# Kernel tuning notes

Hardware: AMD Instinct MI355X
Metric: run time of the kernel (lower is better)

Reference implementation:

```python
import jax, jax.numpy as jnp
import numpy as np

B, T, V = 4, 4096, 1024
NB = 64          # n_basis -> basis dim = 2*NB
C = 256          # n_channels


def setup_inputs() -> dict:
    key = jax.random.key(0)
    ks = jax.random.split(key, 8)
    return {
        "x": jax.random.normal(ks[0], (B, T, V), dtype=jnp.float32),
        "basis": jax.random.normal(ks[1], (V, 2 * NB), dtype=jnp.float32),
        "q_coeffs": jax.random.normal(ks[2], (C, 2 * NB), dtype=jnp.float32) * 0.02,
        "k_coeffs": jax.random.normal(ks[3], (C, 2 * NB), dtype=jnp.float32) * 0.02,
        "v_coeffs": jax.random.normal(ks[4], (C, 2 * NB), dtype=jnp.float32) * 0.02,
        "o_coeffs": jax.random.normal(ks[5], (C, 2 * NB), dtype=jnp.float32) * 0.02,
        "decay_logit": jnp.float32(3.0),
        "out_scale": jnp.float32(0.1),
    }


def reference(x, basis, q_coeffs, k_coeffs, v_coeffs, o_coeffs, decay_logit, out_scale):
    # Fourier projections: [V, 2NB] @ [2NB, C] -> [V, C]
    q_w = basis @ q_coeffs.T
    k_w = basis @ k_coeffs.T
    v_w = basis @ v_coeffs.T
    o_w = basis @ o_coeffs.T

    queries = x @ q_w   # [B,T,C]
    keys = x @ k_w      # [B,T,C]
    values = x @ v_w    # [B,T,C]

    scores = jnp.einsum("btc,bsc->bts", queries, keys)  # [B,T,T]

    decay = jax.nn.sigmoid(decay_logit)
    t = x.shape[1]
    pos = jnp.arange(t)
    diff = pos[None, :] - pos[:, None]          # diff[s,t] = t - s (matches torch)
    causal = (diff > 0).astype(x.dtype)
    decay_weights = (decay ** jnp.maximum(diff - 1, 0).astype(x.dtype)) * causal

    scores = scores * decay_weights[None]       # [B,T,T]
    retrieved = jnp.einsum("bts,bsc->btc", scores, values)  # [B,T,C]
    return (retrieved @ o_w.T) * out_scale      # [B,T,V]
```

## Files before the change

### kernel.cpp

```cpp
#include <hip/hip_runtime.h>


#define Bb 4
#define Tt 4096
#define Vv 1024
#define Ff 128
#define Cc 256
#define TC 64
#define Gg (Tt / TC)
#define QLD 768

typedef __attribute__((ext_vector_type(8))) short short8;
typedef __attribute__((ext_vector_type(4))) float f32x4;

__device__ __forceinline__ float dsigmoid(const float* p) {
    return 1.0f / (1.0f + expf(-p[0]));
}
__device__ __forceinline__ ushort f2bf(float f) {
    unsigned u = __float_as_uint(f);
    u = (u + 0x7FFFu + ((u >> 16) & 1u)) >> 16;
    return (ushort)u;
}
__device__ __forceinline__ float bf2f(ushort u) {
    return __uint_as_float(((unsigned)u) << 16);
}

__global__ __launch_bounds__(256) void prep_weights(
    const float* __restrict__ basis, const float* __restrict__ qc,
    const float* __restrict__ kc, const float* __restrict__ vc,
    const float* __restrict__ oc,
    ushort* __restrict__ basisTb,
    ushort* __restrict__ qkvc,
    ushort* __restrict__ ocb)
{
    int i = blockIdx.x * 256 + threadIdx.x;
    if (i < Ff * Vv) {
        int f = i >> 10, v = i & 1023;
        basisTb[i] = f2bf(basis[v * Ff + f]);
    }
    if (i < 768 * Ff) {
        int ch = i >> 7, f = i & 127;
        const float* src = ch < 256 ? qc : (ch < 512 ? kc : vc);
        qkvc[i] = f2bf(src[(ch & 255) * Ff + f]);
    }
    if (i < Cc * Ff) ocb[i] = f2bf(oc[i]);
}

template<int AMODE, int OMODE>
__global__ __launch_bounds__(256) void mgemm(
    const void* __restrict__ Ap, const ushort* __restrict__ Bt,
    void* __restrict__ Cp, int N_total, int K_total, int ldA, int Ksplit,
    const float* __restrict__ alpha_ptr)
{
    __shared__ ushort Asm[128][40];
    __shared__ ushort Bsm[128][40];
    const int tid = threadIdx.x;
    const int row0 = blockIdx.x * 128;
    const int col0 = blockIdx.y * 128;
    const int kb = blockIdx.z * Ksplit;

    const int trow = tid >> 1;
    const int thalf = (tid & 1) * 16;

    const int l = tid & 63, w = tid >> 6;
    const int wr = (w >> 1) * 64, wc = (w & 1) * 64;
    const int lrow = l & 15, lk = l >> 4;

    f32x4 acc[4][4];
#pragma unroll
    for (int mi = 0; mi < 4; ++mi)
#pragma unroll
        for (int ni = 0; ni < 4; ++ni) {
            f32x4 z = {0.f, 0.f, 0.f, 0.f};
            acc[mi][ni] = z;
        }

    for (int k0 = kb; k0 < kb + Ksplit; k0 += 32) {
        if (AMODE == 1) {
            const float* ap = (const float*)Ap + (size_t)(row0 + trow) * ldA + k0 + thalf;
            float4 f0 = ((const float4*)ap)[0];
            float4 f1 = ((const float4*)ap)[1];
            float4 f2 = ((const float4*)ap)[2];
            float4 f3 = ((const float4*)ap)[3];
            union { ushort us[16]; int4 i4[2]; } t;
            t.us[0] = f2bf(f0.x); t.us[1] = f2bf(f0.y); t.us[2] = f2bf(f0.z); t.us[3] = f2bf(f0.w);
            t.us[4] = f2bf(f1.x); t.us[5] = f2bf(f1.y); t.us[6] = f2bf(f1.z); t.us[7] = f2bf(f1.w);
            t.us[8] = f2bf(f2.x); t.us[9] = f2bf(f2.y); t.us[10] = f2bf(f2.z); t.us[11] = f2bf(f2.w);
            t.us[12] = f2bf(f3.x); t.us[13] = f2bf(f3.y); t.us[14] = f2bf(f3.z); t.us[15] = f2bf(f3.w);
            *(int4*)&Asm[trow][thalf] = t.i4[0];
            *(int4*)&Asm[trow][thalf + 8] = t.i4[1];
        } else {
            const ushort* ap = (const ushort*)Ap + (size_t)(row0 + trow) * ldA + k0 + thalf;
            *(int4*)&Asm[trow][thalf] = ((const int4*)ap)[0];
            *(int4*)&Asm[trow][thalf + 8] = ((const int4*)ap)[1];
        }
        {
            const ushort* bp = Bt + (size_t)(col0 + trow) * K_total + k0 + thalf;
            *(int4*)&Bsm[trow][thalf] = ((const int4*)bp)[0];
            *(int4*)&Bsm[trow][thalf + 8] = ((const int4*)bp)[1];
        }
        __syncthreads();
        short8 af[4], bf[4];
#pragma unroll
        for (int mi = 0; mi < 4; ++mi)
            af[mi] = *(const short8*)&Asm[wr + mi * 16 + lrow][lk * 8];
#pragma unroll
        for (int ni = 0; ni < 4; ++ni)
            bf[ni] = *(const short8*)&Bsm[wc + ni * 16 + lrow][lk * 8];
#pragma unroll
        for (int mi = 0; mi < 4; ++mi)
#pragma unroll
            for (int ni = 0; ni < 4; ++ni)
                acc[mi][ni] = __builtin_amdgcn_mfma_f32_16x16x32_bf16(
                    af[mi], bf[ni], acc[mi][ni], 0, 0, 0);
        __syncthreads();
    }

    const float alpha = (OMODE == 1) ? alpha_ptr[0] : 1.0f;
    size_t slab = (OMODE == 2) ? (size_t)blockIdx.z * (size_t)gridDim.x * 128 * N_total : 0;
#pragma unroll
    for (int mi = 0; mi < 4; ++mi) {
#pragma unroll
        for (int ni = 0; ni < 4; ++ni) {
#pragma unroll
            for (int r = 0; r < 4; ++r) {
                int row = row0 + wr + mi * 16 + lk * 4 + r;
                int col = col0 + wc + ni * 16 + lrow;
                size_t idx = slab + (size_t)row * N_total + col;
                if (OMODE == 0) ((ushort*)Cp)[idx] = f2bf(acc[mi][ni][r]);
                else ((float*)Cp)[idx] = acc[mi][ni][r] * alpha;
            }
        }
    }
}

__global__ __launch_bounds__(256) void reduce_xb(
    const float* __restrict__ p, ushort* __restrict__ xb)
{
    int i = blockIdx.x * 256 + threadIdx.x;
    float4 a = ((const float4*)p)[i];
    float4 b = ((const float4*)(p + (size_t)Bb * Tt * Ff))[i];
    ushort4 o;
    o.x = f2bf(a.x + b.x); o.y = f2bf(a.y + b.y);
    o.z = f2bf(a.z + b.z); o.w = f2bf(a.w + b.w);
    ((ushort4*)xb)[i] = o;
}

__global__ __launch_bounds__(256) void transpose_kv(
    const ushort* __restrict__ qkv, ushort* __restrict__ Kts,
    ushort* __restrict__ Vt, const float* __restrict__ dlogit)
{
    __shared__ ushort tile[64][72];
    __shared__ float dp[64];
    const int tid = threadIdx.x;
    const int t0 = blockIdx.x * 64, c0 = blockIdx.y * 64;
    const int b = blockIdx.z >> 1, mat = blockIdx.z & 1;
    const float d = dsigmoid(dlogit);
    if (tid < 64) dp[tid] = powf(d, (float)tid);
    const int coff = 256 + mat * 256 + c0;
#pragma unroll
    for (int j = 0; j < 2; ++j) {
        int row = (tid >> 3) + j * 32;
        int seg = (tid & 7) * 8;
        *(int4*)&tile[row][seg] =
            *(const int4*)(qkv + ((size_t)(b * Tt + t0 + row)) * QLD + coff + seg);
    }
    __syncthreads();
    const int cl = tid & 63, tb = (tid >> 6) * 16;
    ushort* outp = (mat ? Vt : Kts) + ((size_t)(b * Cc + c0 + cl)) * Tt + t0 + tb;
#pragma unroll
    for (int h = 0; h < 2; ++h) {
        union { ushort us[8]; int4 v; } o;
#pragma unroll
        for (int jj = 0; jj < 8; ++jj) {
            int tl = tb + h * 8 + jj;
            ushort val = tile[tl][cl];
            if (mat == 0) val = f2bf(bf2f(val) * dp[tl]);
            o.us[jj] = val;
        }
        *(int4*)(outp + h * 8) = o.v;
    }
}

__global__ __launch_bounds__(256) void chunk_lt(
    const ushort* __restrict__ Kts, const ushort* __restrict__ Vt,
    ushort* __restrict__ LT)
{
    const int tid = threadIdx.x;
    const int g = blockIdx.y, b = blockIdx.z;
    const int c0 = (blockIdx.x & 1) * 128, cp0 = (blockIdx.x >> 1) * 128;
    const int w = tid >> 6, l = tid & 63;
    const int wc = (w >> 1) * 64, wcp = (w & 1) * 64;
    const int lrow = l & 15, lk = l >> 4;

    f32x4 acc[4][4];
#pragma unroll
    for (int mi = 0; mi < 4; ++mi)
#pragma unroll
        for (int ni = 0; ni < 4; ++ni) {
            f32x4 z = {0.f, 0.f, 0.f, 0.f};
            acc[mi][ni] = z;
        }
#pragma unroll
    for (int ks = 0; ks < 2; ++ks) {
        short8 af[4], bf[4];
#pragma unroll
        for (int mi = 0; mi < 4; ++mi)
            af[mi] = *(const short8*)(Vt +
                ((size_t)(b * Cc + c0 + wc + mi * 16 + lrow)) * Tt + g * TC + ks * 32 + lk * 8);
#pragma unroll
        for (int ni = 0; ni < 4; ++ni)
            bf[ni] = *(const short8*)(Kts +
                ((size_t)(b * Cc + cp0 + wcp + ni * 16 + lrow)) * Tt + g * TC + ks * 32 + lk * 8);
#pragma unroll
        for (int mi = 0; mi < 4; ++mi)
#pragma unroll
            for (int ni = 0; ni < 4; ++ni)
                acc[mi][ni] = __builtin_amdgcn_mfma_f32_16x16x32_bf16(
                    af[mi], bf[ni], acc[mi][ni], 0, 0, 0);
    }
    ushort* lb = LT + (((size_t)(b * Gg + g)) << 16);
#pragma unroll
    for (int mi = 0; mi < 4; ++mi)
#pragma unroll
        for (int ni = 0; ni < 4; ++ni)
#pragma unroll
            for (int r = 0; r < 4; ++r)
                lb[(size_t)(c0 + wc + mi * 16 + lk * 4 + r) * Cc + cp0 + wcp + ni * 16 + lrow]
                    = f2bf(acc[mi][ni][r]);
}

__global__ __launch_bounds__(64) void scan_kernel(
    const ushort* __restrict__ LT, ushort* __restrict__ SbT,
    const float* __restrict__ dlogit)
{
    const int e = blockIdx.x * 64 + threadIdx.x;
    const int b = blockIdx.y;
    const float d = dsigmoid(dlogit);
    const float dTc = powf(d, (float)TC);
    const size_t CC = (size_t)Cc * Cc;
    const size_t base = (size_t)b * Gg * CC + e;
    SbT[base + (size_t)(Gg - 1) * CC] = 0;
    float cur = 0.f;
    ushort nxt = LT[base + (size_t)(Gg - 1) * CC];
    for (int g = Gg - 2; g >= 0; --g) {
        float L = bf2f(nxt);
        if (g > 0) nxt = LT[base + (size_t)g * CC];
        cur = L + dTc * cur;
        SbT[base + (size_t)g * CC] = f2bf(cur);
    }
}

__global__ __launch_bounds__(256) void attn_mfma(
    const ushort* __restrict__ qkv, const ushort* __restrict__ SbT,
    const ushort* __restrict__ Vt, ushort* __restrict__ retrb,
    const float* __restrict__ dlogit)
{
    __shared__ ushort Qsm[64][264];
    __shared__ ushort Ksm[64][264];
    __shared__ ushort Psm[64][72];
    __shared__ float dpow[64];
    const int tid = threadIdx.x;
    const int g = blockIdx.x, b = blockIdx.y;
    const float d = dsigmoid(dlogit);
    if (tid < 64) dpow[tid] = powf(d, (float)tid);

    const ushort* qb = qkv + ((size_t)(b * Tt + g * TC)) * QLD;
#pragma unroll
    for (int j = 0; j < 8; ++j) {
        int seg = tid + 256 * j;
        int row = seg >> 5, sc = (seg & 31) * 8;
        *(int4*)&Qsm[row][sc] = *(const int4*)(qb + (size_t)row * QLD + sc);
        *(int4*)&Ksm[row][sc] = *(const int4*)(qb + (size_t)row * QLD + 256 + sc);
    }
    __syncthreads();

    const int w = tid >> 6, l = tid & 63;
    const int lrow = l & 15, lk = l >> 4;

    f32x4 acc1[4];
#pragma unroll
    for (int mi = 0; mi < 4; ++mi) { f32x4 z = {0.f,0.f,0.f,0.f}; acc1[mi] = z; }
#pragma unroll
    for (int ks = 0; ks < 8; ++ks) {
        short8 bf = *(const short8*)&Ksm[w * 16 + lrow][ks * 32 + lk * 8];
#pragma unroll
        for (int mi = 0; mi < 4; ++mi) {
            short8 af = *(const short8*)&Qsm[mi * 16 + lrow][ks * 32 + lk * 8];
            acc1[mi] = __builtin_amdgcn_mfma_f32_16x16x32_bf16(af, bf, acc1[mi], 0, 0, 0);
        }
    }
#pragma unroll
    for (int mi = 0; mi < 4; ++mi)
#pragma unroll
        for (int r = 0; r < 4; ++r) {
            int t = mi * 16 + lk * 4 + r, s = w * 16 + lrow;
            float p = (s > t) ? acc1[mi][r] * dpow[s - t - 1] : 0.f;
            Psm[t][s] = f2bf(p);
        }
    __syncthreads();

    f32x4 acc[4][4];
#pragma unroll
    for (int mi = 0; mi < 4; ++mi)
#pragma unroll
        for (int ni = 0; ni < 4; ++ni) {
            f32x4 z = {0.f, 0.f, 0.f, 0.f};
            acc[mi][ni] = z;
        }

    const ushort* Sg = SbT + (((size_t)(b * Gg + g)) << 16);
#pragma unroll
    for (int ks = 0; ks < 8; ++ks) {
        short8 af[4], bf[4];
#pragma unroll
        for (int mi = 0; mi < 4; ++mi)
            af[mi] = *(const short8*)&Qsm[mi * 16 + lrow][ks * 32 + lk * 8];
#pragma unroll
        for (int ni = 0; ni < 4; ++ni)
            bf[ni] = *(const short8*)(Sg +
                (size_t)(w * 64 + ni * 16 + lrow) * Cc + ks * 32 + lk * 8);
#pragma unroll
        for (int mi = 0; mi < 4; ++mi)
#pragma unroll
            for (int ni = 0; ni < 4; ++ni)
                acc[mi][ni] = __builtin_amdgcn_mfma_f32_16x16x32_bf16(
                    af[mi], bf[ni], acc[mi][ni], 0, 0, 0);
    }
#pragma unroll
    for (int mi = 0; mi < 4; ++mi) {
#pragma unroll
        for (int r = 0; r < 4; ++r) {
            float wq = dpow[63 - (mi * 16 + lk * 4 + r)];
#pragma unroll
            for (int ni = 0; ni < 4; ++ni) acc[mi][ni][r] *= wq;
        }
    }
#pragma unroll
    for (int ks = 0; ks < 2; ++ks) {
        short8 af[4], bf[4];
#pragma unroll
        for (int mi = 0; mi < 4; ++mi)
            af[mi] = *(const short8*)&Psm[mi * 16 + lrow][ks * 32 + lk * 8];
#pragma unroll
        for (int ni = 0; ni < 4; ++ni)
            bf[ni] = *(const short8*)(Vt +
                ((size_t)(b * Cc + w * 64 + ni * 16 + lrow)) * Tt + g * TC + ks * 32 + lk * 8);
#pragma unroll
        for (int mi = 0; mi < 4; ++mi)
#pragma unroll
            for (int ni = 0; ni < 4; ++ni)
                acc[mi][ni] = __builtin_amdgcn_mfma_f32_16x16x32_bf16(
                    af[mi], bf[ni], acc[mi][ni], 0, 0, 0);
    }

    ushort* rb = retrb + ((size_t)(b * Tt + g * TC)) * Cc;
#pragma unroll
    for (int mi = 0; mi < 4; ++mi)
#pragma unroll
        for (int ni = 0; ni < 4; ++ni)
#pragma unroll
            for (int r = 0; r < 4; ++r)
                rb[(size_t)(mi * 16 + lk * 4 + r) * Cc + w * 64 + ni * 16 + lrow]
                    = f2bf(acc[mi][ni][r]);
}

extern "C" void kernel_launch(void* const* d_in, const int* in_sizes, int n_in,
                              void* d_out, int out_size, void* d_ws, size_t ws_size,
                              hipStream_t stream) {
    const float* x      = (const float*)d_in[0];
    const float* basis  = (const float*)d_in[1];
    const float* qc     = (const float*)d_in[2];
    const float* kc     = (const float*)d_in[3];
    const float* vc     = (const float*)d_in[4];
    const float* oc     = (const float*)d_in[5];
    const float* dlogit = (const float*)d_in[6];
    const float* oscale = (const float*)d_in[7];
    float* out = (float*)d_out;

    char* w = (char*)d_ws;
    ushort* basisTb = (ushort*)w;  w += (size_t)Ff * Vv * 2;
    ushort* qkvc    = (ushort*)w;  w += (size_t)768 * Ff * 2;
    ushort* ocb     = (ushort*)w;  w += (size_t)Cc * Ff * 2;
    ushort* ow      = (ushort*)w;  w += (size_t)Vv * Cc * 2;
    float*  xbp     = (float*)w;   w += (size_t)2 * Bb * Tt * Ff * 4;
    ushort* xb      = (ushort*)w;  w += (size_t)Bb * Tt * Ff * 2;
    ushort* qkv     = (ushort*)w;  w += (size_t)Bb * Tt * QLD * 2;
    ushort* Kts     = (ushort*)w;  w += (size_t)Bb * Cc * Tt * 2;
    ushort* Vt      = (ushort*)w;  w += (size_t)Bb * Cc * Tt * 2;
    ushort* LT      = (ushort*)w;  w += (size_t)Bb * Gg * Cc * Cc * 2;
    ushort* SbT     = (ushort*)w;  w += (size_t)Bb * Gg * Cc * Cc * 2;
    ushort* retrb   = (ushort*)w;  w += (size_t)Bb * Tt * Cc * 2;

    prep_weights<<<512, 256, 0, stream>>>(basis, qc, kc, vc, oc, basisTb, qkvc, ocb);
    mgemm<1, 0><<<dim3(8, 2), 256, 0, stream>>>(basis, ocb, ow, Cc, Ff, Ff, Ff, nullptr);
    mgemm<1, 2><<<dim3(128, 1, 2), 256, 0, stream>>>(x, basisTb, xbp, Ff, Vv, Vv, 512, nullptr);
    reduce_xb<<<2048, 256, 0, stream>>>(xbp, xb);
    mgemm<0, 0><<<dim3(128, 6), 256, 0, stream>>>(xb, qkvc, qkv, QLD, Ff, Ff, Ff, nullptr);
    transpose_kv<<<dim3(Tt / 64, Cc / 64, Bb * 2), 256, 0, stream>>>(qkv, Kts, Vt, dlogit);
    chunk_lt<<<dim3(4, Gg, Bb), 256, 0, stream>>>(Kts, Vt, LT);
    scan_kernel<<<dim3(Cc * Cc / 64, Bb), 64, 0, stream>>>(LT, SbT, dlogit);
    attn_mfma<<<dim3(Gg, Bb), 256, 0, stream>>>(qkv, SbT, Vt, retrb, dlogit);
    mgemm<0, 1><<<dim3(128, 8), 256, 0, stream>>>(retrb, ow, out, Vv, Cc, Cc, Cc, oscale);
}
```

Baseline: 243.1 us.

## Double-buffer GEMM LDS tiles and widen split-K with bf16 partials

The shared GEMM kernel now double-buffers its LDS tiles: the next K-tile is loaded into registers while MFMAs run on the current one, which drops one barrier per iteration. The x@basis projection goes from split-K of 2 to split-K of 8, raising the block count from 256 to 1024 to better fill the GPU. Its partial sums are stored as bf16 in the reused LT buffer and summed by a vectorised reduce kernel. This cuts partial-sum traffic and workspace but adds bf16 rounding to each partial before the reduction.

```diff
diff --git a/kernel.cpp b/kernel.cpp
--- a/kernel.cpp
+++ b/kernel.cpp
@@ -52,12 +52,13 @@
     void* __restrict__ Cp, int N_total, int K_total, int ldA, int Ksplit,
     const float* __restrict__ alpha_ptr)
 {
-    __shared__ ushort Asm[128][40];
-    __shared__ ushort Bsm[128][40];
+    __shared__ ushort Asm[2][128][40];
+    __shared__ ushort Bsm[2][128][40];
     const int tid = threadIdx.x;
     const int row0 = blockIdx.x * 128;
     const int col0 = blockIdx.y * 128;
     const int kb = blockIdx.z * Ksplit;
+    const int kend = kb + Ksplit;
 
     const int trow = tid >> 1;
     const int thalf = (tid & 1) * 16;
@@ -75,49 +76,71 @@
             acc[mi][ni] = z;
         }
 
-    for (int k0 = kb; k0 < kb + Ksplit; k0 += 32) {
-        if (AMODE == 1) {
-            const float* ap = (const float*)Ap + (size_t)(row0 + trow) * ldA + k0 + thalf;
-            float4 f0 = ((const float4*)ap)[0];
-            float4 f1 = ((const float4*)ap)[1];
-            float4 f2 = ((const float4*)ap)[2];
-            float4 f3 = ((const float4*)ap)[3];
-            union { ushort us[16]; int4 i4[2]; } t;
-            t.us[0] = f2bf(f0.x); t.us[1] = f2bf(f0.y); t.us[2] = f2bf(f0.z); t.us[3] = f2bf(f0.w);
-            t.us[4] = f2bf(f1.x); t.us[5] = f2bf(f1.y); t.us[6] = f2bf(f1.z); t.us[7] = f2bf(f1.w);
-            t.us[8] = f2bf(f2.x); t.us[9] = f2bf(f2.y); t.us[10] = f2bf(f2.z); t.us[11] = f2bf(f2.w);
-            t.us[12] = f2bf(f3.x); t.us[13] = f2bf(f3.y); t.us[14] = f2bf(f3.z); t.us[15] = f2bf(f3.w);
-            *(int4*)&Asm[trow][thalf] = t.i4[0];
-            *(int4*)&Asm[trow][thalf + 8] = t.i4[1];
-        } else {
-            const ushort* ap = (const ushort*)Ap + (size_t)(row0 + trow) * ldA + k0 + thalf;
-            *(int4*)&Asm[trow][thalf] = ((const int4*)ap)[0];
-            *(int4*)&Asm[trow][thalf + 8] = ((const int4*)ap)[1];
-        }
-        {
-            const ushort* bp = Bt + (size_t)(col0 + trow) * K_total + k0 + thalf;
-            *(int4*)&Bsm[trow][thalf] = ((const int4*)bp)[0];
-            *(int4*)&Bsm[trow][thalf + 8] = ((const int4*)bp)[1];
-        }
+    float4 fa0, fa1, fa2, fa3;
+    int4 ia0, ia1;
+    int4 ib0, ib1;
+
+#define LOAD_TILE(K0)                                                              \
+    do {                                                                           \
+        if (AMODE == 1) {                                                          \
+            const float* ap = (const float*)Ap + (size_t)(row0 + trow) * ldA + (K0) + thalf; \
+            fa0 = ((const float4*)ap)[0]; fa1 = ((const float4*)ap)[1];            \
+            fa2 = ((const float4*)ap)[2]; fa3 = ((const float4*)ap)[3];            \
+        } else {                                                                   \
+            const ushort* ap = (const ushort*)Ap + (size_t)(row0 + trow) * ldA + (K0) + thalf; \
+            ia0 = ((const int4*)ap)[0]; ia1 = ((const int4*)ap)[1];                \
+        }                                                                          \
+        const ushort* bp = Bt + (size_t)(col0 + trow) * K_total + (K0) + thalf;    \
+        ib0 = ((const int4*)bp)[0]; ib1 = ((const int4*)bp)[1];                    \
+    } while (0)
+
+#define STORE_TILE(BUF)                                                            \
+    do {                                                                           \
+        if (AMODE == 1) {                                                          \
+            union { ushort us[16]; int4 i4[2]; } t;                                \
+            t.us[0] = f2bf(fa0.x); t.us[1] = f2bf(fa0.y); t.us[2] = f2bf(fa0.z); t.us[3] = f2bf(fa0.w); \
+            t.us[4] = f2bf(fa1.x); t.us[5] = f2bf(fa1.y); t.us[6] = f2bf(fa1.z); t.us[7] = f2bf(fa1.w); \
+            t.us[8] = f2bf(fa2.x); t.us[9] = f2bf(fa2.y); t.us[10] = f2bf(fa2.z); t.us[11] = f2bf(fa2.w); \
+            t.us[12] = f2bf(fa3.x); t.us[13] = f2bf(fa3.y); t.us[14] = f2bf(fa3.z); t.us[15] = f2bf(fa3.w); \
+            *(int4*)&Asm[BUF][trow][thalf] = t.i4[0];                              \
+            *(int4*)&Asm[BUF][trow][thalf + 8] = t.i4[1];                          \
+        } else {                                                                   \
+            *(int4*)&Asm[BUF][trow][thalf] = ia0;                                  \
+            *(int4*)&Asm[BUF][trow][thalf + 8] = ia1;                              \
+        }                                                                          \
+        *(int4*)&Bsm[BUF][trow][thalf] = ib0;                                      \
+        *(int4*)&Bsm[BUF][trow][thalf + 8] = ib1;                                  \
+    } while (0)
+
+    LOAD_TILE(kb);
+    STORE_TILE(0);
+    int cur = 0;
+
+    for (int k0 = kb; k0 < kend; k0 += 32) {
         __syncthreads();
+        const bool more = (k0 + 32 < kend);
+        if (more) LOAD_TILE(k0 + 32);
         short8 af[4], bf[4];
 #pragma unroll
         for (int mi = 0; mi < 4; ++mi)
-            af[mi] = *(const short8*)&Asm[wr + mi * 16 + lrow][lk * 8];
-#pragma unroll
-        for (int ni = 0; ni < 4; ++ni)
-            bf[ni] = *(const short8*)&Bsm[wc + ni * 16 + lrow][lk * 8];
+            af[mi] = *(const short8*)&Asm[cur][wr + mi * 16 + lrow][lk * 8];
+#pragma unroll
+        for (int ni = 0; ni < 4; ++ni)
+            bf[ni] = *(const short8*)&Bsm[cur][wc + ni * 16 + lrow][lk * 8];
 #pragma unroll
         for (int mi = 0; mi < 4; ++mi)
 #pragma unroll
             for (int ni = 0; ni < 4; ++ni)
                 acc[mi][ni] = __builtin_amdgcn_mfma_f32_16x16x32_bf16(
                     af[mi], bf[ni], acc[mi][ni], 0, 0, 0);
-        __syncthreads();
-    }
+        if (more) STORE_TILE(cur ^ 1);
+        cur ^= 1;
+    }
+#undef LOAD_TILE
+#undef STORE_TILE
 
     const float alpha = (OMODE == 1) ? alpha_ptr[0] : 1.0f;
-    size_t slab = (OMODE == 2) ? (size_t)blockIdx.z * (size_t)gridDim.x * 128 * N_total : 0;
+    size_t slab = (OMODE == 3) ? (size_t)blockIdx.z * (size_t)gridDim.x * 128 * N_total : 0;
 #pragma unroll
     for (int mi = 0; mi < 4; ++mi) {
 #pragma unroll
@@ -127,23 +150,30 @@
                 int row = row0 + wr + mi * 16 + lk * 4 + r;
                 int col = col0 + wc + ni * 16 + lrow;
                 size_t idx = slab + (size_t)row * N_total + col;
-                if (OMODE == 0) ((ushort*)Cp)[idx] = f2bf(acc[mi][ni][r]);
-                else ((float*)Cp)[idx] = acc[mi][ni][r] * alpha;
+                if (OMODE == 1) ((float*)Cp)[idx] = acc[mi][ni][r] * alpha;
+                else ((ushort*)Cp)[idx] = f2bf(acc[mi][ni][r]);
             }
         }
     }
 }
 
 __global__ __launch_bounds__(256) void reduce_xb(
-    const float* __restrict__ p, ushort* __restrict__ xb)
-{
-    int i = blockIdx.x * 256 + threadIdx.x;
-    float4 a = ((const float4*)p)[i];
-    float4 b = ((const float4*)(p + (size_t)Bb * Tt * Ff))[i];
-    ushort4 o;
-    o.x = f2bf(a.x + b.x); o.y = f2bf(a.y + b.y);
-    o.z = f2bf(a.z + b.z); o.w = f2bf(a.w + b.w);
-    ((ushort4*)xb)[i] = o;
+    const ushort* __restrict__ p, ushort* __restrict__ xb)
+{
+    const size_t SLAB = (size_t)Bb * Tt * Ff;
+    size_t i = ((size_t)blockIdx.x * 256 + threadIdx.x) * 8;
+    float s[8] = {0.f, 0.f, 0.f, 0.f, 0.f, 0.f, 0.f, 0.f};
+#pragma unroll
+    for (int z = 0; z < 8; ++z) {
+        union { int4 v; ushort us[8]; } t;
+        t.v = *(const int4*)(p + z * SLAB + i);
+#pragma unroll
+        for (int j = 0; j < 8; ++j) s[j] += bf2f(t.us[j]);
+    }
+    union { int4 v; ushort us[8]; } o;
+#pragma unroll
+    for (int j = 0; j < 8; ++j) o.us[j] = f2bf(s[j]);
+    *(int4*)(xb + i) = o.v;
 }
 
 __global__ __launch_bounds__(256) void transpose_kv(
@@ -383,7 +413,6 @@
     ushort* qkvc    = (ushort*)w;  w += (size_t)768 * Ff * 2;
     ushort* ocb     = (ushort*)w;  w += (size_t)Cc * Ff * 2;
     ushort* ow      = (ushort*)w;  w += (size_t)Vv * Cc * 2;
-    float*  xbp     = (float*)w;   w += (size_t)2 * Bb * Tt * Ff * 4;
     ushort* xb      = (ushort*)w;  w += (size_t)Bb * Tt * Ff * 2;
     ushort* qkv     = (ushort*)w;  w += (size_t)Bb * Tt * QLD * 2;
     ushort* Kts     = (ushort*)w;  w += (size_t)Bb * Cc * Tt * 2;
@@ -391,11 +420,12 @@
     ushort* LT      = (ushort*)w;  w += (size_t)Bb * Gg * Cc * Cc * 2;
     ushort* SbT     = (ushort*)w;  w += (size_t)Bb * Gg * Cc * Cc * 2;
     ushort* retrb   = (ushort*)w;  w += (size_t)Bb * Tt * Cc * 2;
+    ushort* xbp     = LT;
 
     prep_weights<<<512, 256, 0, stream>>>(basis, qc, kc, vc, oc, basisTb, qkvc, ocb);
     mgemm<1, 0><<<dim3(8, 2), 256, 0, stream>>>(basis, ocb, ow, Cc, Ff, Ff, Ff, nullptr);
-    mgemm<1, 2><<<dim3(128, 1, 2), 256, 0, stream>>>(x, basisTb, xbp, Ff, Vv, Vv, 512, nullptr);
-    reduce_xb<<<2048, 256, 0, stream>>>(xbp, xb);
+    mgemm<1, 3><<<dim3(128, 1, 8), 256, 0, stream>>>(x, basisTb, xbp, Ff, Vv, Vv, 128, nullptr);
+    reduce_xb<<<1024, 256, 0, stream>>>(xbp, xb);
     mgemm<0, 0><<<dim3(128, 6), 256, 0, stream>>>(xb, qkvc, qkv, QLD, Ff, Ff, Ff, nullptr);
     transpose_kv<<<dim3(Tt / 64, Cc / 64, Bb * 2), 256, 0, stream>>>(qkv, Kts, Vt, dlogit);
     chunk_lt<<<dim3(4, Gg, Bb), 256, 0, stream>>>(Kts, Vt, LT);
```

New measurement: 248.3 us. +2.1%, slower.

## Fold basis into QKV weights and use direct-to-LDS bf16 GEMM

Applied to the files above, without the earlier changes.

Instead of projecting x onto the 128-dim basis with a split-K GEMM, a reduction, and a second GEMM, it precomputes the combined 768x1024 QKV weight (coeffs @ basis^T) and runs one GEMM from a bf16 copy of x. A new kernel converts x to bf16 up front. The GEMM kernel now loads tiles with global_load_lds and uses K=64 steps with unpadded LDS rows, which may cause bank conflicts. The scan is unrolled by four to batch loads, and the LT buffer aliases the x bf16 buffer. The change trades the x->basis intermediate for a larger K=1024 GEMM producing qkv directly, and double-rounding behaviour differs.

```diff
diff --git a/kernel.cpp b/kernel.cpp
--- a/kernel.cpp
+++ b/kernel.cpp
@@ -24,44 +24,56 @@
 __device__ __forceinline__ float bf2f(ushort u) {
     return __uint_as_float(((unsigned)u) << 16);
 }
+__device__ __forceinline__ void gl_lds16(ushort* lds, const ushort* gp) {
+    __builtin_amdgcn_global_load_lds(
+        (const __attribute__((address_space(1))) unsigned int*)gp,
+        (__attribute__((address_space(3))) unsigned int*)lds,
+        16, 0, 0);
+}
+
+__global__ __launch_bounds__(256) void convert_x(
+    const float* __restrict__ x, ushort* __restrict__ xbf)
+{
+    const size_t total = (size_t)Bb * Tt * Vv;
+    for (size_t i = ((size_t)blockIdx.x * 256 + threadIdx.x) * 8; i < total;
+         i += (size_t)2048 * 256 * 8) {
+        float4 a = *(const float4*)(x + i);
+        float4 b = *(const float4*)(x + i + 4);
+        union { ushort us[8]; int4 v; } o;
+        o.us[0] = f2bf(a.x); o.us[1] = f2bf(a.y); o.us[2] = f2bf(a.z); o.us[3] = f2bf(a.w);
+        o.us[4] = f2bf(b.x); o.us[5] = f2bf(b.y); o.us[6] = f2bf(b.z); o.us[7] = f2bf(b.w);
+        *(int4*)(xbf + i) = o.v;
+    }
+}
 
 __global__ __launch_bounds__(256) void prep_weights(
     const float* __restrict__ basis, const float* __restrict__ qc,
     const float* __restrict__ kc, const float* __restrict__ vc,
     const float* __restrict__ oc,
-    ushort* __restrict__ basisTb,
+    ushort* __restrict__ basisb,
     ushort* __restrict__ qkvc,
     ushort* __restrict__ ocb)
 {
     int i = blockIdx.x * 256 + threadIdx.x;
-    if (i < Ff * Vv) {
-        int f = i >> 10, v = i & 1023;
-        basisTb[i] = f2bf(basis[v * Ff + f]);
-    }
+    if (i < Vv * Ff) basisb[i] = f2bf(basis[i]);
     if (i < 768 * Ff) {
-        int ch = i >> 7, f = i & 127;
+        int ch = i >> 7;
         const float* src = ch < 256 ? qc : (ch < 512 ? kc : vc);
-        qkvc[i] = f2bf(src[(ch & 255) * Ff + f]);
+        qkvc[i] = f2bf(src[(ch & 255) * Ff + (i & 127)]);
     }
     if (i < Cc * Ff) ocb[i] = f2bf(oc[i]);
 }
 
-template<int AMODE, int OMODE>
-__global__ __launch_bounds__(256) void mgemm(
-    const void* __restrict__ Ap, const ushort* __restrict__ Bt,
-    void* __restrict__ Cp, int N_total, int K_total, int ldA, int Ksplit,
+template<int OMODE>
+__global__ __launch_bounds__(256) void ggemm(
+    const ushort* __restrict__ A, const ushort* __restrict__ Bt,
+    void* __restrict__ Cp, int N_total, int K_total, int ldA,
     const float* __restrict__ alpha_ptr)
 {
-    __shared__ ushort Asm[128][40];
-    __shared__ ushort Bsm[128][40];
+    __shared__ ushort Asm[128 * 64];
+    __shared__ ushort Bsm[128 * 64];
     const int tid = threadIdx.x;
-    const int row0 = blockIdx.x * 128;
-    const int col0 = blockIdx.y * 128;
-    const int kb = blockIdx.z * Ksplit;
-
-    const int trow = tid >> 1;
-    const int thalf = (tid & 1) * 16;
-
+    const int row0 = blockIdx.x * 128, col0 = blockIdx.y * 128;
     const int l = tid & 63, w = tid >> 6;
     const int wr = (w >> 1) * 64, wc = (w & 1) * 64;
     const int lrow = l & 15, lk = l >> 4;
@@ -75,75 +87,47 @@
             acc[mi][ni] = z;
         }
 
-    for (int k0 = kb; k0 < kb + Ksplit; k0 += 32) {
-        if (AMODE == 1) {
-            const float* ap = (const float*)Ap + (size_t)(row0 + trow) * ldA + k0 + thalf;
-            float4 f0 = ((const float4*)ap)[0];
-            float4 f1 = ((const float4*)ap)[1];
-            float4 f2 = ((const float4*)ap)[2];
-            float4 f3 = ((const float4*)ap)[3];
-            union { ushort us[16]; int4 i4[2]; } t;
-            t.us[0] = f2bf(f0.x); t.us[1] = f2bf(f0.y); t.us[2] = f2bf(f0.z); t.us[3] = f2bf(f0.w);
-            t.us[4] = f2bf(f1.x); t.us[5] = f2bf(f1.y); t.us[6] = f2bf(f1.z); t.us[7] = f2bf(f1.w);
-            t.us[8] = f2bf(f2.x); t.us[9] = f2bf(f2.y); t.us[10] = f2bf(f2.z); t.us[11] = f2bf(f2.w);
-            t.us[12] = f2bf(f3.x); t.us[13] = f2bf(f3.y); t.us[14] = f2bf(f3.z); t.us[15] = f2bf(f3.w);
-            *(int4*)&Asm[trow][thalf] = t.i4[0];
-            *(int4*)&Asm[trow][thalf + 8] = t.i4[1];
-        } else {
-            const ushort* ap = (const ushort*)Ap + (size_t)(row0 + trow) * ldA + k0 + thalf;
-            *(int4*)&Asm[trow][thalf] = ((const int4*)ap)[0];
-            *(int4*)&Asm[trow][thalf + 8] = ((const int4*)ap)[1];
-        }
-        {
-            const ushort* bp = Bt + (size_t)(col0 + trow) * K_total + k0 + thalf;
-            *(int4*)&Bsm[trow][thalf] = ((const int4*)bp)[0];
-            *(int4*)&Bsm[trow][thalf + 8] = ((const int4*)bp)[1];
+    for (int k0 = 0; k0 < K_total; k0 += 64) {
+#pragma unroll
+        for (int call = 0; call < 4; ++call) {
+            int ia = tid * 8 + call * 2048;
+            int r = ia >> 6, c = ia & 63;
+            gl_lds16(&Asm[ia], A + (size_t)(row0 + r) * ldA + k0 + c);
+            gl_lds16(&Bsm[ia], Bt + (size_t)(col0 + r) * K_total + k0 + c);
         }
         __syncthreads();
-        short8 af[4], bf[4];
-#pragma unroll
-        for (int mi = 0; mi < 4; ++mi)
-            af[mi] = *(const short8*)&Asm[wr + mi * 16 + lrow][lk * 8];
-#pragma unroll
-        for (int ni = 0; ni < 4; ++ni)
-            bf[ni] = *(const short8*)&Bsm[wc + ni * 16 + lrow][lk * 8];
-#pragma unroll
-        for (int mi = 0; mi < 4; ++mi)
+#pragma unroll
+        for (int ks = 0; ks < 2; ++ks) {
+            short8 af[4], bf[4];
+#pragma unroll
+            for (int mi = 0; mi < 4; ++mi)
+                af[mi] = *(const short8*)&Asm[(wr + mi * 16 + lrow) * 64 + ks * 32 + lk * 8];
 #pragma unroll
             for (int ni = 0; ni < 4; ++ni)
-                acc[mi][ni] = __builtin_amdgcn_mfma_f32_16x16x32_bf16(
-                    af[mi], bf[ni], acc[mi][ni], 0, 0, 0);
+                bf[ni] = *(const short8*)&Bsm[(wc + ni * 16 + lrow) * 64 + ks * 32 + lk * 8];
+#pragma unroll
+            for (int mi = 0; mi < 4; ++mi)
+#pragma unroll
+                for (int ni = 0; ni < 4; ++ni)
+                    acc[mi][ni] = __builtin_amdgcn_mfma_f32_16x16x32_bf16(
+                        af[mi], bf[ni], acc[mi][ni], 0, 0, 0);
+        }
         __syncthreads();
     }
 
     const float alpha = (OMODE == 1) ? alpha_ptr[0] : 1.0f;
-    size_t slab = (OMODE == 2) ? (size_t)blockIdx.z * (size_t)gridDim.x * 128 * N_total : 0;
-#pragma unroll
-    for (int mi = 0; mi < 4; ++mi) {
-#pragma unroll
-        for (int ni = 0; ni < 4; ++ni) {
+#pragma unroll
+    for (int mi = 0; mi < 4; ++mi)
+#pragma unroll
+        for (int ni = 0; ni < 4; ++ni)
 #pragma unroll
             for (int r = 0; r < 4; ++r) {
                 int row = row0 + wr + mi * 16 + lk * 4 + r;
                 int col = col0 + wc + ni * 16 + lrow;
-                size_t idx = slab + (size_t)row * N_total + col;
-                if (OMODE == 0) ((ushort*)Cp)[idx] = f2bf(acc[mi][ni][r]);
-                else ((float*)Cp)[idx] = acc[mi][ni][r] * alpha;
+                size_t idx = (size_t)row * N_total + col;
+                if (OMODE == 1) ((float*)Cp)[idx] = acc[mi][ni][r] * alpha;
+                else ((ushort*)Cp)[idx] = f2bf(acc[mi][ni][r]);
             }
-        }
-    }
-}
-
-__global__ __launch_bounds__(256) void reduce_xb(
-    const float* __restrict__ p, ushort* __restrict__ xb)
-{
-    int i = blockIdx.x * 256 + threadIdx.x;
-    float4 a = ((const float4*)p)[i];
-    float4 b = ((const float4*)(p + (size_t)Bb * Tt * Ff))[i];
-    ushort4 o;
-    o.x = f2bf(a.x + b.x); o.y = f2bf(a.y + b.y);
-    o.z = f2bf(a.z + b.z); o.w = f2bf(a.w + b.w);
-    ((ushort4*)xb)[i] = o;
 }
 
 __global__ __launch_bounds__(256) void transpose_kv(
@@ -242,12 +226,20 @@
     const size_t base = (size_t)b * Gg * CC + e;
     SbT[base + (size_t)(Gg - 1) * CC] = 0;
     float cur = 0.f;
-    ushort nxt = LT[base + (size_t)(Gg - 1) * CC];
-    for (int g = Gg - 2; g >= 0; --g) {
-        float L = bf2f(nxt);
-        if (g > 0) nxt = LT[base + (size_t)g * CC];
-        cur = L + dTc * cur;
-        SbT[base + (size_t)g * CC] = f2bf(cur);
+    int j = Gg - 1;
+    for (; j >= 4; j -= 4) {
+        ushort l0 = LT[base + (size_t)j * CC];
+        ushort l1 = LT[base + (size_t)(j - 1) * CC];
+        ushort l2 = LT[base + (size_t)(j - 2) * CC];
+        ushort l3 = LT[base + (size_t)(j - 3) * CC];
+        cur = bf2f(l0) + dTc * cur; SbT[base + (size_t)(j - 1) * CC] = f2bf(cur);
+        cur = bf2f(l1) + dTc * cur; SbT[base + (size_t)(j - 2) * CC] = f2bf(cur);
+        cur = bf2f(l2) + dTc * cur; SbT[base + (size_t)(j - 3) * CC] = f2bf(cur);
+        cur = bf2f(l3) + dTc * cur; SbT[base + (size_t)(j - 4) * CC] = f2bf(cur);
+    }
+    for (; j >= 1; --j) {
+        cur = bf2f(LT[base + (size_t)j * CC]) + dTc * cur;
+        SbT[base + (size_t)(j - 1) * CC] = f2bf(cur);
     }
 }
 
@@ -379,27 +371,27 @@
     float* out = (float*)d_out;
 
     char* w = (char*)d_ws;
-    ushort* basisTb = (ushort*)w;  w += (size_t)Ff * Vv * 2;
+    ushort* basisb  = (ushort*)w;  w += (size_t)Vv * Ff * 2;
     ushort* qkvc    = (ushort*)w;  w += (size_t)768 * Ff * 2;
     ushort* ocb     = (ushort*)w;  w += (size_t)Cc * Ff * 2;
     ushort* ow      = (ushort*)w;  w += (size_t)Vv * Cc * 2;
-    float*  xbp     = (float*)w;   w += (size_t)2 * Bb * Tt * Ff * 4;
-    ushort* xb      = (ushort*)w;  w += (size_t)Bb * Tt * Ff * 2;
+    ushort* Wq      = (ushort*)w;  w += (size_t)768 * Vv * 2;
+    ushort* xbf     = (ushort*)w;  w += (size_t)Bb * Tt * Vv * 2;
     ushort* qkv     = (ushort*)w;  w += (size_t)Bb * Tt * QLD * 2;
     ushort* Kts     = (ushort*)w;  w += (size_t)Bb * Cc * Tt * 2;
     ushort* Vt      = (ushort*)w;  w += (size_t)Bb * Cc * Tt * 2;
-    ushort* LT      = (ushort*)w;  w += (size_t)Bb * Gg * Cc * Cc * 2;
     ushort* SbT     = (ushort*)w;  w += (size_t)Bb * Gg * Cc * Cc * 2;
     ushort* retrb   = (ushort*)w;  w += (size_t)Bb * Tt * Cc * 2;
-
-    prep_weights<<<512, 256, 0, stream>>>(basis, qc, kc, vc, oc, basisTb, qkvc, ocb);
-    mgemm<1, 0><<<dim3(8, 2), 256, 0, stream>>>(basis, ocb, ow, Cc, Ff, Ff, Ff, nullptr);
-    mgemm<1, 2><<<dim3(128, 1, 2), 256, 0, stream>>>(x, basisTb, xbp, Ff, Vv, Vv, 512, nullptr);
-    reduce_xb<<<2048, 256, 0, stream>>>(xbp, xb);
-    mgemm<0, 0><<<dim3(128, 6), 256, 0, stream>>>(xb, qkvc, qkv, QLD, Ff, Ff, Ff, nullptr);
+    ushort* LT      = xbf;
+
+    convert_x<<<2048, 256, 0, stream>>>(x, xbf);
+    prep_weights<<<512, 256, 0, stream>>>(basis, qc, kc, vc, oc, basisb, qkvc, ocb);
+    ggemm<0><<<dim3(6, 8), 256, 0, stream>>>(qkvc, basisb, Wq, Vv, Ff, Ff, nullptr);
+    ggemm<0><<<dim3(8, 2), 256, 0, stream>>>(basisb, ocb, ow, Cc, Ff, Ff, nullptr);
+    ggemm<0><<<dim3(128, 6), 256, 0, stream>>>(xbf, Wq, qkv, QLD, Vv, Vv, nullptr);
     transpose_kv<<<dim3(Tt / 64, Cc / 64, Bb * 2), 256, 0, stream>>>(qkv, Kts, Vt, dlogit);
     chunk_lt<<<dim3(4, Gg, Bb), 256, 0, stream>>>(Kts, Vt, LT);
     scan_kernel<<<dim3(Cc * Cc / 64, Bb), 64, 0, stream>>>(LT, SbT, dlogit);
     attn_mfma<<<dim3(Gg, Bb), 256, 0, stream>>>(qkv, SbT, Vt, retrb, dlogit);
-    mgemm<0, 1><<<dim3(128, 8), 256, 0, stream>>>(retrb, ow, out, Vv, Cc, Cc, Cc, oscale);
-}
+    ggemm<1><<<dim3(128, 8), 256, 0, stream>>>(retrb, ow, out, Vv, Cc, Cc, oscale);
+}
```

Result: slower. 270.7 us (+11.3%).
